# Kernel optimization log

Measured on AMD Instinct MI355X. Metric: run time of the kernel, lower is better.

## Reference

```python
import jax, jax.numpy as jnp
import numpy as np
from jax import lax

D = 1024  # input_dim
H = 1024  # hidden_dim
N = 32
T = 512


def setup_inputs() -> dict:
    key = jax.random.key(0)
    k1, k2, k3, k4 = jax.random.split(key, 4)
    std = 1.0 / np.sqrt(D + H)
    x = jax.random.normal(k1, (N, T, D), dtype=jnp.float32)
    state = jax.random.normal(k2, (N, H), dtype=jnp.float32)
    weight = jax.random.normal(k3, (D + H, 3 * (D + H)), dtype=jnp.float32) * std
    bias = jax.random.normal(k4, (3 * (D + H),), dtype=jnp.float32) * std
    return {"x": x, "state": state, "weight": weight, "bias": bias}


def reference(x, state, weight, bias):
    # weight slices, matching get_weights()
    Wxt = weight[:D, : 3 * H]            # (D, 3H)
    Wxd = weight[:D, 3 * H :]            # (D, 3D)
    Whd = weight[D:, 3 * H :]            # (H, 3D)
    Whtg = weight[D:, : 2 * H]           # (H, 2H)
    Whtc = weight[D:, 2 * H : 3 * H]     # (H, H)

    # temporal pre-activations: (N, T, 3H)
    gates = jnp.einsum('ntd,dk->ntk', x, Wxt) + bias[: 3 * H]

    def step(prev_ht, g_t):
        # g_t: (N, 3H)
        gg = jax.nn.sigmoid(g_t[:, : 2 * H] + prev_ht @ Whtg)
        u = gg[:, :H]
        r = gg[:, H:]
        hc = jnp.tanh(g_t[:, 2 * H :] + (r * prev_ht) @ Whtc)
        ht = prev_ht + u * (hc - prev_ht)
        return ht, ht

    final_ht, ht_seq = lax.scan(step, state, jnp.swapaxes(gates, 0, 1))
    ht = jnp.swapaxes(ht_seq, 0, 1)  # (N, T, H)

    # depth gates: bias + ht @ Whd everywhere; +x @ Wxd only on gate part
    gd = jnp.einsum('nth,hk->ntk', ht, Whd) + bias[3 * H :]       # (N, T, 3D)
    g2 = jax.nn.sigmoid(gd[..., : 2 * D] + jnp.einsum('ntd,dk->ntk', x, Wxd[:, : 2 * D]))
    ud = g2[..., :D]
    rd = g2[..., D:]
    hcd = jnp.tanh(gd[..., 2 * D :] + jnp.einsum('ntd,dk->ntk', rd * x, Wxd[:, 2 * D :]))
    h = x + ud * (hcd - x)
    return h, final_ht
```

## Files before the change

### kernel.cpp

```cpp
#include <hip/hip_runtime.h>
#include <cstdint>
#include <cstddef>

typedef unsigned int uint;
typedef unsigned short ushort;
typedef unsigned long long u64;
typedef __attribute__((ext_vector_type(8))) __bf16 bf16x8;
typedef __attribute__((ext_vector_type(4))) __bf16 bf16x4v;
typedef __attribute__((ext_vector_type(4))) float floatx4;

#define WLD 6144

static const size_t OFF_GATES = 0;
static const size_t OFF_XB    = 100663296;
static const size_t OFF_HTSEQ = 134217728;
static const size_t OFF_WHTGT = OFF_HTSEQ;
static const size_t OFF_WHTCT = OFF_HTSEQ + 4194304;
static const size_t OFF_WXTT  = 167772160;
static const size_t OFF_COMM  = OFF_WXTT;
static const size_t OFF_WHDT  = 174063616;
static const size_t OFF_WXD1T = 180355072;
static const size_t OFF_WXD2T = 184549376;

__device__ __forceinline__ float sigmoidf_(float x) { return 1.f / (1.f + __expf(-x)); }
__device__ __forceinline__ float tanhf_(float x) { float e = __expf(2.f * x); return 1.f - 2.f / (e + 1.f); }

__device__ __forceinline__ u64 ald64(const u64* p) {
  return __hip_atomic_load(p, __ATOMIC_RELAXED, __HIP_MEMORY_SCOPE_AGENT);
}
__device__ __forceinline__ void ast64(u64* p, u64 v) {
  __hip_atomic_store(p, v, __ATOMIC_RELAXED, __HIP_MEMORY_SCOPE_AGENT);
}
__device__ __forceinline__ ushort bfb(float v) {
  union { __bf16 b; ushort u; } t; t.b = (__bf16)v; return t.u;
}
__device__ __forceinline__ u64 pack4(float v) {
  ushort h = bfb(v);
  uint p2 = (uint)h | ((uint)(ushort)__shfl_xor((int)h, 1) << 16);
  u64 p4 = (u64)p2 | ((u64)(uint)__shfl_xor((int)p2, 2) << 32);
  return p4;
}


__global__ __launch_bounds__(256) void convert_x(const float4* __restrict__ x4,
                                                 __bf16* __restrict__ xb) {
  const int s = blockIdx.x;
  const int n = s >> 9, t = s & 511;
  const int d = (t << 5) | n;
  float4 v = x4[(size_t)s * 256 + threadIdx.x];
  bf16x4v o = { (__bf16)v.x, (__bf16)v.y, (__bf16)v.z, (__bf16)v.w };
  *reinterpret_cast<bf16x4v*>(xb + (size_t)d * 1024 + threadIdx.x * 4) = o;
}

__global__ __launch_bounds__(256) void zero_flags(u64* __restrict__ f) {
  ast64(f + (size_t)blockIdx.x * 256 + threadIdx.x, 0ull);
}

__global__ __launch_bounds__(256) void transpose_conv(const float* __restrict__ src,
                                                      __bf16* __restrict__ dst) {
  __shared__ float t[32][33];
  const int ct = blockIdx.x, kt = blockIdx.y;
  const int j = threadIdx.x & 31, ig = threadIdx.x >> 5;
#pragma unroll
  for (int ii = 0; ii < 4; ++ii) {
    int i = ig * 4 + ii;
    t[i][j] = src[(size_t)(kt * 32 + i) * WLD + ct * 32 + j];
  }
  __syncthreads();
#pragma unroll
  for (int ii = 0; ii < 4; ++ii) {
    int cc = ig * 4 + ii;
    dst[(size_t)(ct * 32 + cc) * 1024 + kt * 32 + j] = (__bf16)t[j][cc];
  }
}

template <int MODE>
__global__ __launch_bounds__(256) void gemm_bt(const __bf16* __restrict__ A, int lda,
                                               const __bf16* __restrict__ BT,
                                               const float* __restrict__ bias,
                                               __bf16* __restrict__ gbuf,
                                               const float* __restrict__ xf,
                                               float* __restrict__ hout, int ncols) {
  __shared__ __bf16 As[128][48];
  __shared__ __bf16 Bs[128][48];
  const int tid = threadIdx.x;
  const int lane = tid & 63, wave = tid >> 6;
  const int tm = blockIdx.y, tn = blockIdx.x;
  const int wm = (wave & 1) * 64, wn = (wave >> 1) * 64;
  floatx4 acc[4][4] = {};
  const int c = tid & 3, r0 = tid >> 2;
  const size_t arow = (size_t)tm * 128;
  const size_t brow = (size_t)tn * 128;

  for (int kk = 0; kk < 1024; kk += 32) {
    *reinterpret_cast<uint4*>(&As[r0][c * 8]) =
        *reinterpret_cast<const uint4*>(A + (arow + r0) * (size_t)lda + kk + c * 8);
    *reinterpret_cast<uint4*>(&As[r0 + 64][c * 8]) =
        *reinterpret_cast<const uint4*>(A + (arow + r0 + 64) * (size_t)lda + kk + c * 8);
    *reinterpret_cast<uint4*>(&Bs[r0][c * 8]) =
        *reinterpret_cast<const uint4*>(BT + (brow + r0) * 1024 + kk + c * 8);
    *reinterpret_cast<uint4*>(&Bs[r0 + 64][c * 8]) =
        *reinterpret_cast<const uint4*>(BT + (brow + r0 + 64) * 1024 + kk + c * 8);
    __syncthreads();
    const int mr = lane & 15, kg = (lane >> 4) * 8;
    bf16x8 af[4], bfr[4];
#pragma unroll
    for (int f = 0; f < 4; ++f) af[f] = *reinterpret_cast<const bf16x8*>(&As[wm + f * 16 + mr][kg]);
#pragma unroll
    for (int f = 0; f < 4; ++f) bfr[f] = *reinterpret_cast<const bf16x8*>(&Bs[wn + f * 16 + mr][kg]);
#pragma unroll
    for (int fi = 0; fi < 4; ++fi)
#pragma unroll
      for (int fj = 0; fj < 4; ++fj)
        acc[fi][fj] = __builtin_amdgcn_mfma_f32_16x16x32_bf16(af[fi], bfr[fj], acc[fi][fj], 0, 0, 0);
    __syncthreads();
  }

#pragma unroll
  for (int fi = 0; fi < 4; ++fi)
#pragma unroll
    for (int fj = 0; fj < 4; ++fj) {
      const int row0 = tm * 128 + wm + fi * 16 + (lane >> 4) * 4;
      const int col = tn * 128 + wn + fj * 16 + (lane & 15);
#pragma unroll
      for (int r = 0; r < 4; ++r) {
        const size_t row = (size_t)(row0 + r);
        float v = acc[fi][fj][r];
        if (MODE == 0 || MODE == 1) {
          gbuf[row * 3072 + col] = (__bf16)(v + bias[col]);
        } else if (MODE == 2) {
          float g = sigmoidf_(v + (float)gbuf[row * 3072 + col]);
          const size_t xrow = (size_t)(row & 31) * 512 + (row >> 5);
          if (col < 1024)
            gbuf[row * 3072 + col] = (__bf16)g;
          else
            gbuf[row * 3072 + col] = (__bf16)(g * xf[xrow * 1024 + (col - 1024)]);
        } else {
          float hcd = tanhf_(v + (float)gbuf[row * 3072 + 2048 + col]);
          float ud = (float)gbuf[row * 3072 + col];
          const size_t xrow = (size_t)(row & 31) * 512 + (row >> 5);
          float xv = xf[xrow * 1024 + col];
          hout[xrow * 1024 + col] = xv + ud * (hcd - xv);
        }
      }
    }
}

#define SMEM_BYTES 136960
#define WS 1032
__global__ __launch_bounds__(512) void recur_kernel(
    const __bf16* __restrict__ gates, const float* __restrict__ state,
    const __bf16* __restrict__ whtg_t, const __bf16* __restrict__ whtc_t,
    u64* __restrict__ ht_w, u64* __restrict__ rh_w,
    u64* __restrict__ fht, u64* __restrict__ frh,
    __bf16* __restrict__ htseq, float* __restrict__ otail) {
  extern __shared__ char smem[];
  __bf16* Wg  = (__bf16*)smem;
  __bf16* Wc  = (__bf16*)(smem + 66048);
  float*  red = (float*)(smem + 99072);
  float*  u_s = (float*)(smem + 132864);
  float*  hp_s= (float*)(smem + 134912);

  const int b = blockIdx.x, tid = threadIdx.x;
  const int lane = tid & 63, w = tid >> 6;
  const int mr = lane & 15, kq = lane >> 4;
  const int base0 = mr * 256 + w * 32 + kq * 2;
  const int base1 = (16 + mr) * 256 + w * 32 + kq * 2;

  for (int idx = tid; idx < 4096; idx += 512) {
    int row = idx >> 7, seg = idx & 127;
    int src = (row < 16) ? (b * 16 + row) : (1024 + b * 16 + row - 16);
    *reinterpret_cast<uint4*>(Wg + row * WS + seg * 8) =
        *reinterpret_cast<const uint4*>(whtg_t + (size_t)src * 1024 + seg * 8);
  }
  for (int idx = tid; idx < 2048; idx += 512) {
    int row = idx >> 7, seg = idx & 127;
    *reinterpret_cast<uint4*>(Wc + row * WS + seg * 8) =
        *reinterpret_cast<const uint4*>(whtc_t + (size_t)(b * 16 + row) * 1024 + seg * 8);
  }
  {
    int n = tid >> 4, cc = tid & 15;
    float sv = state[n * 1024 + b * 16 + cc];
    hp_s[n * 16 + cc] = sv;
    u64 p4 = pack4(sv);
    if (!(cc & 3)) ast64(ht_w + 8192 + n * 256 + b * 4 + (cc >> 2), p4);
  }
  __syncthreads();
  if (tid == 0) {
    asm volatile("s_waitcnt vmcnt(0)" ::: "memory");
    ast64(fht + b * 16, 1ull);
  }

  for (int t = 0; t < 512; ++t) {
    const uint e = (uint)t + 1u;
    const u64* htb = ht_w + (size_t)(e & 1) * 8192;
    u64*       rhb = rh_w + (size_t)(e & 1) * 8192;
    float hn_keep = 0.f;
    {
      __bf16 graw0, graw1;
      {
        int n = tid >> 5, col = tid & 31;
        int cc = (col < 16) ? (b * 16 + col) : (1024 + b * 16 + col - 16);
        graw0 = gates[(size_t)(t * 32 + n) * 3072 + cc];
        int o2 = tid + 512, n2 = o2 >> 5;
        graw1 = gates[(size_t)(t * 32 + n2) * 3072 + cc];
      }
      {
        const u64* fp = fht + (size_t)(w * 8 + (lane & 7)) * 16;
        bool rdy;
        do {
          u64 v = (lane < 8) ? ald64(fp) : (u64)e;
          rdy = (v >= (u64)e);
        } while (!__all(rdy));
        asm volatile("" ::: "memory");
      }
      u64 wa[4][2], wb[4][2];
#pragma unroll
      for (int c2 = 0; c2 < 4; ++c2) {
        wa[c2][0] = ald64(htb + base0 + c2 * 8);
        wa[c2][1] = ald64(htb + base0 + c2 * 8 + 1);
        wb[c2][0] = ald64(htb + base1 + c2 * 8);
        wb[c2][1] = ald64(htb + base1 + c2 * 8 + 1);
      }
      floatx4 acc[2][2] = {};
#pragma unroll
      for (int c2 = 0; c2 < 4; ++c2) {
        union { uint4 u; bf16x8 v; } fa, fb;
        fa.u = make_uint4((uint)wa[c2][0], (uint)(wa[c2][0] >> 32),
                          (uint)wa[c2][1], (uint)(wa[c2][1] >> 32));
        fb.u = make_uint4((uint)wb[c2][0], (uint)(wb[c2][0] >> 32),
                          (uint)wb[c2][1], (uint)(wb[c2][1] >> 32));
        const int kb = w * 128 + c2 * 32 + kq * 8;
        bf16x8 b0 = *reinterpret_cast<const bf16x8*>(Wg + mr * WS + kb);
        bf16x8 b1 = *reinterpret_cast<const bf16x8*>(Wg + (16 + mr) * WS + kb);
        acc[0][0] = __builtin_amdgcn_mfma_f32_16x16x32_bf16(fa.v, b0, acc[0][0], 0, 0, 0);
        acc[0][1] = __builtin_amdgcn_mfma_f32_16x16x32_bf16(fa.v, b1, acc[0][1], 0, 0, 0);
        acc[1][0] = __builtin_amdgcn_mfma_f32_16x16x32_bf16(fb.v, b0, acc[1][0], 0, 0, 0);
        acc[1][1] = __builtin_amdgcn_mfma_f32_16x16x32_bf16(fb.v, b1, acc[1][1], 0, 0, 0);
      }
#pragma unroll
      for (int ai = 0; ai < 2; ++ai)
#pragma unroll
        for (int cj = 0; cj < 2; ++cj)
#pragma unroll
          for (int r = 0; r < 4; ++r)
            red[w * 1056 + (ai * 16 + kq * 4 + r) * 33 + cj * 16 + mr] = acc[ai][cj][r];
      __syncthreads();
      {
        int n = tid >> 5, col = tid & 31;
        float s = 0.f;
#pragma unroll
        for (int w8 = 0; w8 < 8; ++w8) s += red[w8 * 1056 + n * 33 + col];
        float gg = sigmoidf_(s + (float)graw0);
        float pub = (col >= 16) ? gg * hp_s[n * 16 + (col - 16)] : 0.f;
        if (col < 16) u_s[n * 16 + col] = gg;
        u64 p4 = pack4(pub);
        if (col >= 16 && !(col & 3))
          ast64(rhb + n * 256 + b * 4 + ((col - 16) >> 2), p4);
        int o2 = tid + 512, n2 = o2 >> 5;
        float s2 = 0.f;
#pragma unroll
        for (int w8 = 0; w8 < 8; ++w8) s2 += red[w8 * 1056 + n2 * 33 + col];
        float gg2 = sigmoidf_(s2 + (float)graw1);
        float pub2 = (col >= 16) ? gg2 * hp_s[n2 * 16 + (col - 16)] : 0.f;
        if (col < 16) u_s[n2 * 16 + col] = gg2;
        u64 p42 = pack4(pub2);
        if (col >= 16 && !(col & 3))
          ast64(rhb + n2 * 256 + b * 4 + ((col - 16) >> 2), p42);
      }
      __syncthreads();
      if (tid == 0) {
        asm volatile("s_waitcnt vmcnt(0)" ::: "memory");
        ast64(frh + b * 16, (u64)e);
      }
    }
    {
      __bf16 gcraw;
      {
        int n = tid >> 4, col = tid & 15;
        gcraw = gates[(size_t)(t * 32 + n) * 3072 + 2048 + b * 16 + col];
      }
      {
        const u64* fp = frh + (size_t)(w * 8 + (lane & 7)) * 16;
        bool rdy;
        do {
          u64 v = (lane < 8) ? ald64(fp) : (u64)e;
          rdy = (v >= (u64)e);
        } while (!__all(rdy));
        asm volatile("" ::: "memory");
      }
      u64 wa[4][2], wb[4][2];
#pragma unroll
      for (int c2 = 0; c2 < 4; ++c2) {
        wa[c2][0] = ald64(rhb + base0 + c2 * 8);
        wa[c2][1] = ald64(rhb + base0 + c2 * 8 + 1);
        wb[c2][0] = ald64(rhb + base1 + c2 * 8);
        wb[c2][1] = ald64(rhb + base1 + c2 * 8 + 1);
      }
      floatx4 acc[2] = {};
#pragma unroll
      for (int c2 = 0; c2 < 4; ++c2) {
        union { uint4 u; bf16x8 v; } fa, fb;
        fa.u = make_uint4((uint)wa[c2][0], (uint)(wa[c2][0] >> 32),
                          (uint)wa[c2][1], (uint)(wa[c2][1] >> 32));
        fb.u = make_uint4((uint)wb[c2][0], (uint)(wb[c2][0] >> 32),
                          (uint)wb[c2][1], (uint)(wb[c2][1] >> 32));
        const int kb = w * 128 + c2 * 32 + kq * 8;
        bf16x8 bb = *reinterpret_cast<const bf16x8*>(Wc + mr * WS + kb);
        acc[0] = __builtin_amdgcn_mfma_f32_16x16x32_bf16(fa.v, bb, acc[0], 0, 0, 0);
        acc[1] = __builtin_amdgcn_mfma_f32_16x16x32_bf16(fb.v, bb, acc[1], 0, 0, 0);
      }
#pragma unroll
      for (int ai = 0; ai < 2; ++ai)
#pragma unroll
        for (int r = 0; r < 4; ++r)
          red[w * 1056 + (ai * 16 + kq * 4 + r) * 33 + mr] = acc[ai][r];
      __syncthreads();
      {
        int n = tid >> 4, col = tid & 15;
        float s = 0.f;
#pragma unroll
        for (int w8 = 0; w8 < 8; ++w8) s += red[w8 * 1056 + n * 33 + col];
        float hc = tanhf_(s + (float)gcraw);
        float hp = hp_s[n * 16 + col];
        float uu = u_s[n * 16 + col];
        float hn = hp + uu * (hc - hp);
        hp_s[n * 16 + col] = hn;
        hn_keep = hn;
        u64 p4 = pack4(hn);
        if (!(col & 3))
          ast64(ht_w + (size_t)((e + 1u) & 1) * 8192 + n * 256 + b * 4 + (col >> 2), p4);
      }
      __syncthreads();
      if (tid == 0) {
        asm volatile("s_waitcnt vmcnt(0)" ::: "memory");
        ast64(fht + b * 16, (u64)(e + 1u));
      }
      {
        int n = tid >> 4, col = tid & 15;
        htseq[(size_t)(t * 32 + n) * 1024 + b * 16 + col] = (__bf16)hn_keep;
        if (t == 511) otail[n * 1024 + b * 16 + col] = hn_keep;
      }
    }
  }
}


extern "C" void kernel_launch(void* const* d_in, const int* in_sizes, int n_in,
                              void* d_out, int out_size, void* d_ws, size_t ws_size,
                              hipStream_t stream) {
  const float* x = (const float*)d_in[0];
  const float* state = (const float*)d_in[1];
  const float* weight = (const float*)d_in[2];
  const float* bias = (const float*)d_in[3];
  float* out = (float*)d_out;
  char* ws = (char*)d_ws;

  __bf16* gates  = (__bf16*)(ws + OFF_GATES);
  __bf16* xb     = (__bf16*)(ws + OFF_XB);
  __bf16* htseq  = (__bf16*)(ws + OFF_HTSEQ);
  __bf16* whtg_t = (__bf16*)(ws + OFF_WHTGT);
  __bf16* whtc_t = (__bf16*)(ws + OFF_WHTCT);
  __bf16* wxtt   = (__bf16*)(ws + OFF_WXTT);
  __bf16* whdt   = (__bf16*)(ws + OFF_WHDT);
  __bf16* wxd1t  = (__bf16*)(ws + OFF_WXD1T);
  __bf16* wxd2t  = (__bf16*)(ws + OFF_WXD2T);
  u64*    comm   = (u64*)(ws + OFF_COMM);
  u64*    ht_w   = comm;
  u64*    rh_w   = comm + 16384;
  u64*    fht    = comm + 32768;
  u64*    frh    = comm + 33792;

  hipLaunchKernelGGL(convert_x, dim3(16384), dim3(256), 0, stream, (const float4*)x, xb);
  hipLaunchKernelGGL(transpose_conv, dim3(96, 32), dim3(256), 0, stream, weight, wxtt);
  hipLaunchKernelGGL(transpose_conv, dim3(64, 32), dim3(256), 0, stream, weight + 3072, wxd1t);
  hipLaunchKernelGGL(transpose_conv, dim3(32, 32), dim3(256), 0, stream, weight + 5120, wxd2t);
  hipLaunchKernelGGL(transpose_conv, dim3(96, 32), dim3(256), 0, stream,
                     weight + (size_t)1024 * WLD + 3072, whdt);
  hipLaunchKernelGGL(transpose_conv, dim3(64, 32), dim3(256), 0, stream,
                     weight + (size_t)1024 * WLD, whtg_t);
  hipLaunchKernelGGL(transpose_conv, dim3(32, 32), dim3(256), 0, stream,
                     weight + (size_t)1024 * WLD + 2048, whtc_t);

  hipLaunchKernelGGL((gemm_bt<0>), dim3(24, 128), dim3(256), 0, stream,
                     xb, 1024, wxtt, bias, gates, (const float*)nullptr, (float*)nullptr, 3072);

  hipLaunchKernelGGL(zero_flags, dim3(8), dim3(256), 0, stream, fht);

  {
    (void)hipFuncSetAttribute(reinterpret_cast<const void*>(recur_kernel),
                              hipFuncAttributeMaxDynamicSharedMemorySize, SMEM_BYTES);
    const __bf16* gatesc = gates;
    float* otail = out + 16777216;
    void* args[10];
    args[0] = (void*)&gatesc; args[1] = (void*)&state;  args[2] = (void*)&whtg_t;
    args[3] = (void*)&whtc_t; args[4] = (void*)&ht_w;   args[5] = (void*)&rh_w;
    args[6] = (void*)&fht;    args[7] = (void*)&frh;    args[8] = (void*)&htseq;
    args[9] = (void*)&otail;
    hipLaunchCooperativeKernel(recur_kernel, dim3(64), dim3(512), args, SMEM_BYTES, stream);
  }

  hipLaunchKernelGGL((gemm_bt<1>), dim3(24, 128), dim3(256), 0, stream,
                     htseq, 1024, whdt, bias + 3072, gates, (const float*)nullptr,
                     (float*)nullptr, 3072);
  hipLaunchKernelGGL((gemm_bt<2>), dim3(16, 128), dim3(256), 0, stream,
                     xb, 1024, wxd1t, bias, gates, x, (float*)nullptr, 2048);
  hipLaunchKernelGGL((gemm_bt<3>), dim3(8, 128), dim3(256), 0, stream,
                     gates + 1024, 3072, wxd2t, bias, gates, x, out, 1024);
}
```

Measured before the change: 6.239 ms.

## Use per-wave completion flags and register state in recurrent kernel

Replaces the per-block flag with per-wave flags, so each wave publishes its slice of h and r*h and signals independently. This removes two block-wide __syncthreads barriers per timestep, and consumers poll all 64 flags of the relevant blocks. Recurrent state (h, u) now lives in registers instead of shared memory. The 64-bit atomic loads are replaced with 128-bit coherent (sc0 sc1) inline-asm loads, and the flag area and zeroing are enlarged. The cost is more flag traffic and polling per step, and correctness now depends on the hand-written asm and explicit waitcnt ordering.

```diff
diff --git a/kernel.cpp b/kernel.cpp
--- a/kernel.cpp
+++ b/kernel.cpp
@@ -39,6 +39,10 @@
   uint p2 = (uint)h | ((uint)(ushort)__shfl_xor((int)h, 1) << 16);
   u64 p4 = (u64)p2 | ((u64)(uint)__shfl_xor((int)p2, 2) << 32);
   return p4;
+}
+union U4 { uint4 u; bf16x8 v; };
+__device__ __forceinline__ void ld16_cp(U4* dst, const u64* p) {
+  asm volatile("global_load_dwordx4 %0, %1, off sc0 sc1" : "=v"(dst->u) : "v"(p));
 }
 
 
@@ -146,7 +150,7 @@
     }
 }
 
-#define SMEM_BYTES 136960
+#define SMEM_BYTES 150272
 #define WS 1032
 __global__ __launch_bounds__(512) void recur_kernel(
     const __bf16* __restrict__ gates, const float* __restrict__ state,
@@ -155,17 +159,20 @@
     u64* __restrict__ fht, u64* __restrict__ frh,
     __bf16* __restrict__ htseq, float* __restrict__ otail) {
   extern __shared__ char smem[];
-  __bf16* Wg  = (__bf16*)smem;
-  __bf16* Wc  = (__bf16*)(smem + 66048);
-  float*  red = (float*)(smem + 99072);
-  float*  u_s = (float*)(smem + 132864);
-  float*  hp_s= (float*)(smem + 134912);
+  __bf16* Wg   = (__bf16*)smem;
+  __bf16* Wc   = (__bf16*)(smem + 66048);
+  float*  redA = (float*)(smem + 99072);
+  float*  redB = (float*)(smem + 132864);
 
   const int b = blockIdx.x, tid = threadIdx.x;
   const int lane = tid & 63, w = tid >> 6;
   const int mr = lane & 15, kq = lane >> 4;
+  const int n = 4 * w + kq;
+  const int c = mr;
   const int base0 = mr * 256 + w * 32 + kq * 2;
   const int base1 = (16 + mr) * 256 + w * 32 + kq * 2;
+  const u64* fpA = fht + ((size_t)(w * 8 + (lane >> 3)) * 8 + (lane & 7)) * 16;
+  const u64* fpB = frh + ((size_t)(w * 8 + (lane >> 3)) * 8 + (lane & 7)) * 16;
 
   for (int idx = tid; idx < 4096; idx += 512) {
     int row = idx >> 7, seg = idx & 127;
@@ -178,65 +185,42 @@
     *reinterpret_cast<uint4*>(Wc + row * WS + seg * 8) =
         *reinterpret_cast<const uint4*>(whtc_t + (size_t)(b * 16 + row) * 1024 + seg * 8);
   }
+  float hp_reg = state[n * 1024 + b * 16 + c];
+  float u_reg = 0.f;
   {
-    int n = tid >> 4, cc = tid & 15;
-    float sv = state[n * 1024 + b * 16 + cc];
-    hp_s[n * 16 + cc] = sv;
-    u64 p4 = pack4(sv);
-    if (!(cc & 3)) ast64(ht_w + 8192 + n * 256 + b * 4 + (cc >> 2), p4);
+    u64 p4 = pack4(hp_reg);
+    if (!(lane & 3)) ast64(ht_w + 8192 + n * 256 + b * 4 + (c >> 2), p4);
   }
   __syncthreads();
-  if (tid == 0) {
-    asm volatile("s_waitcnt vmcnt(0)" ::: "memory");
-    ast64(fht + b * 16, 1ull);
-  }
+  if (lane == 0) ast64(fht + (size_t)(b * 8 + w) * 16, 1ull);
 
   for (int t = 0; t < 512; ++t) {
     const uint e = (uint)t + 1u;
     const u64* htb = ht_w + (size_t)(e & 1) * 8192;
     u64*       rhb = rh_w + (size_t)(e & 1) * 8192;
-    float hn_keep = 0.f;
     {
-      __bf16 graw0, graw1;
-      {
-        int n = tid >> 5, col = tid & 31;
-        int cc = (col < 16) ? (b * 16 + col) : (1024 + b * 16 + col - 16);
-        graw0 = gates[(size_t)(t * 32 + n) * 3072 + cc];
-        int o2 = tid + 512, n2 = o2 >> 5;
-        graw1 = gates[(size_t)(t * 32 + n2) * 3072 + cc];
-      }
-      {
-        const u64* fp = fht + (size_t)(w * 8 + (lane & 7)) * 16;
-        bool rdy;
-        do {
-          u64 v = (lane < 8) ? ald64(fp) : (u64)e;
-          rdy = (v >= (u64)e);
-        } while (!__all(rdy));
-        asm volatile("" ::: "memory");
-      }
-      u64 wa[4][2], wb[4][2];
+      __bf16 graw_u = gates[(size_t)(t * 32 + n) * 3072 + b * 16 + c];
+      __bf16 graw_r = gates[(size_t)(t * 32 + n) * 3072 + 1024 + b * 16 + c];
+      while (!__all(ald64(fpA) >= (u64)e)) {}
+      asm volatile("" ::: "memory");
+      U4 wa[4], wb[4];
 #pragma unroll
       for (int c2 = 0; c2 < 4; ++c2) {
-        wa[c2][0] = ald64(htb + base0 + c2 * 8);
-        wa[c2][1] = ald64(htb + base0 + c2 * 8 + 1);
-        wb[c2][0] = ald64(htb + base1 + c2 * 8);
-        wb[c2][1] = ald64(htb + base1 + c2 * 8 + 1);
-      }
+        ld16_cp(&wa[c2], htb + base0 + c2 * 8);
+        ld16_cp(&wb[c2], htb + base1 + c2 * 8);
+      }
+      asm volatile("s_waitcnt vmcnt(0)" ::: "memory");
+      __builtin_amdgcn_sched_barrier(0);
       floatx4 acc[2][2] = {};
 #pragma unroll
       for (int c2 = 0; c2 < 4; ++c2) {
-        union { uint4 u; bf16x8 v; } fa, fb;
-        fa.u = make_uint4((uint)wa[c2][0], (uint)(wa[c2][0] >> 32),
-                          (uint)wa[c2][1], (uint)(wa[c2][1] >> 32));
-        fb.u = make_uint4((uint)wb[c2][0], (uint)(wb[c2][0] >> 32),
-                          (uint)wb[c2][1], (uint)(wb[c2][1] >> 32));
         const int kb = w * 128 + c2 * 32 + kq * 8;
         bf16x8 b0 = *reinterpret_cast<const bf16x8*>(Wg + mr * WS + kb);
         bf16x8 b1 = *reinterpret_cast<const bf16x8*>(Wg + (16 + mr) * WS + kb);
-        acc[0][0] = __builtin_amdgcn_mfma_f32_16x16x32_bf16(fa.v, b0, acc[0][0], 0, 0, 0);
-        acc[0][1] = __builtin_amdgcn_mfma_f32_16x16x32_bf16(fa.v, b1, acc[0][1], 0, 0, 0);
-        acc[1][0] = __builtin_amdgcn_mfma_f32_16x16x32_bf16(fb.v, b0, acc[1][0], 0, 0, 0);
-        acc[1][1] = __builtin_amdgcn_mfma_f32_16x16x32_bf16(fb.v, b1, acc[1][1], 0, 0, 0);
+        acc[0][0] = __builtin_amdgcn_mfma_f32_16x16x32_bf16(wa[c2].v, b0, acc[0][0], 0, 0, 0);
+        acc[0][1] = __builtin_amdgcn_mfma_f32_16x16x32_bf16(wa[c2].v, b1, acc[0][1], 0, 0, 0);
+        acc[1][0] = __builtin_amdgcn_mfma_f32_16x16x32_bf16(wb[c2].v, b0, acc[1][0], 0, 0, 0);
+        acc[1][1] = __builtin_amdgcn_mfma_f32_16x16x32_bf16(wb[c2].v, b1, acc[1][1], 0, 0, 0);
       }
 #pragma unroll
       for (int ai = 0; ai < 2; ++ai)
@@ -244,102 +228,64 @@
         for (int cj = 0; cj < 2; ++cj)
 #pragma unroll
           for (int r = 0; r < 4; ++r)
-            red[w * 1056 + (ai * 16 + kq * 4 + r) * 33 + cj * 16 + mr] = acc[ai][cj][r];
+            redA[w * 1056 + (ai * 16 + kq * 4 + r) * 33 + cj * 16 + mr] = acc[ai][cj][r];
       __syncthreads();
       {
-        int n = tid >> 5, col = tid & 31;
-        float s = 0.f;
-#pragma unroll
-        for (int w8 = 0; w8 < 8; ++w8) s += red[w8 * 1056 + n * 33 + col];
-        float gg = sigmoidf_(s + (float)graw0);
-        float pub = (col >= 16) ? gg * hp_s[n * 16 + (col - 16)] : 0.f;
-        if (col < 16) u_s[n * 16 + col] = gg;
+        float s1 = 0.f, s2 = 0.f;
+#pragma unroll
+        for (int w8 = 0; w8 < 8; ++w8) {
+          s1 += redA[w8 * 1056 + n * 33 + c];
+          s2 += redA[w8 * 1056 + n * 33 + 16 + c];
+        }
+        u_reg = sigmoidf_(s1 + (float)graw_u);
+        float gg_r = sigmoidf_(s2 + (float)graw_r);
+        float pub = gg_r * hp_reg;
         u64 p4 = pack4(pub);
-        if (col >= 16 && !(col & 3))
-          ast64(rhb + n * 256 + b * 4 + ((col - 16) >> 2), p4);
-        int o2 = tid + 512, n2 = o2 >> 5;
-        float s2 = 0.f;
-#pragma unroll
-        for (int w8 = 0; w8 < 8; ++w8) s2 += red[w8 * 1056 + n2 * 33 + col];
-        float gg2 = sigmoidf_(s2 + (float)graw1);
-        float pub2 = (col >= 16) ? gg2 * hp_s[n2 * 16 + (col - 16)] : 0.f;
-        if (col < 16) u_s[n2 * 16 + col] = gg2;
-        u64 p42 = pack4(pub2);
-        if (col >= 16 && !(col & 3))
-          ast64(rhb + n2 * 256 + b * 4 + ((col - 16) >> 2), p42);
-      }
-      __syncthreads();
-      if (tid == 0) {
-        asm volatile("s_waitcnt vmcnt(0)" ::: "memory");
-        ast64(frh + b * 16, (u64)e);
-      }
+        if (!(lane & 3)) ast64(rhb + n * 256 + b * 4 + (c >> 2), p4);
+      }
+      asm volatile("s_waitcnt vmcnt(0)" ::: "memory");
+      if (lane == 0) ast64(frh + (size_t)(b * 8 + w) * 16, (u64)e);
     }
     {
-      __bf16 gcraw;
-      {
-        int n = tid >> 4, col = tid & 15;
-        gcraw = gates[(size_t)(t * 32 + n) * 3072 + 2048 + b * 16 + col];
-      }
-      {
-        const u64* fp = frh + (size_t)(w * 8 + (lane & 7)) * 16;
-        bool rdy;
-        do {
-          u64 v = (lane < 8) ? ald64(fp) : (u64)e;
-          rdy = (v >= (u64)e);
-        } while (!__all(rdy));
-        asm volatile("" ::: "memory");
-      }
-      u64 wa[4][2], wb[4][2];
+      __bf16 gcraw = gates[(size_t)(t * 32 + n) * 3072 + 2048 + b * 16 + c];
+      while (!__all(ald64(fpB) >= (u64)e)) {}
+      asm volatile("" ::: "memory");
+      U4 wa[4], wb[4];
 #pragma unroll
       for (int c2 = 0; c2 < 4; ++c2) {
-        wa[c2][0] = ald64(rhb + base0 + c2 * 8);
-        wa[c2][1] = ald64(rhb + base0 + c2 * 8 + 1);
-        wb[c2][0] = ald64(rhb + base1 + c2 * 8);
-        wb[c2][1] = ald64(rhb + base1 + c2 * 8 + 1);
-      }
+        ld16_cp(&wa[c2], rhb + base0 + c2 * 8);
+        ld16_cp(&wb[c2], rhb + base1 + c2 * 8);
+      }
+      asm volatile("s_waitcnt vmcnt(0)" ::: "memory");
+      __builtin_amdgcn_sched_barrier(0);
       floatx4 acc[2] = {};
 #pragma unroll
       for (int c2 = 0; c2 < 4; ++c2) {
-        union { uint4 u; bf16x8 v; } fa, fb;
-        fa.u = make_uint4((uint)wa[c2][0], (uint)(wa[c2][0] >> 32),
-                          (uint)wa[c2][1], (uint)(wa[c2][1] >> 32));
-        fb.u = make_uint4((uint)wb[c2][0], (uint)(wb[c2][0] >> 32),
-                          (uint)wb[c2][1], (uint)(wb[c2][1] >> 32));
         const int kb = w * 128 + c2 * 32 + kq * 8;
         bf16x8 bb = *reinterpret_cast<const bf16x8*>(Wc + mr * WS + kb);
-        acc[0] = __builtin_amdgcn_mfma_f32_16x16x32_bf16(fa.v, bb, acc[0], 0, 0, 0);
-        acc[1] = __builtin_amdgcn_mfma_f32_16x16x32_bf16(fb.v, bb, acc[1], 0, 0, 0);
+        acc[0] = __builtin_amdgcn_mfma_f32_16x16x32_bf16(wa[c2].v, bb, acc[0], 0, 0, 0);
+        acc[1] = __builtin_amdgcn_mfma_f32_16x16x32_bf16(wb[c2].v, bb, acc[1], 0, 0, 0);
       }
 #pragma unroll
       for (int ai = 0; ai < 2; ++ai)
 #pragma unroll
         for (int r = 0; r < 4; ++r)
-          red[w * 1056 + (ai * 16 + kq * 4 + r) * 33 + mr] = acc[ai][r];
+          redB[w * 544 + (ai * 16 + kq * 4 + r) * 17 + mr] = acc[ai][r];
       __syncthreads();
       {
-        int n = tid >> 4, col = tid & 15;
         float s = 0.f;
 #pragma unroll
-        for (int w8 = 0; w8 < 8; ++w8) s += red[w8 * 1056 + n * 33 + col];
+        for (int w8 = 0; w8 < 8; ++w8) s += redB[w8 * 544 + n * 17 + c];
         float hc = tanhf_(s + (float)gcraw);
-        float hp = hp_s[n * 16 + col];
-        float uu = u_s[n * 16 + col];
-        float hn = hp + uu * (hc - hp);
-        hp_s[n * 16 + col] = hn;
-        hn_keep = hn;
+        float hn = hp_reg + u_reg * (hc - hp_reg);
+        hp_reg = hn;
         u64 p4 = pack4(hn);
-        if (!(col & 3))
-          ast64(ht_w + (size_t)((e + 1u) & 1) * 8192 + n * 256 + b * 4 + (col >> 2), p4);
-      }
-      __syncthreads();
-      if (tid == 0) {
+        if (!(lane & 3))
+          ast64(ht_w + (size_t)((e + 1u) & 1) * 8192 + n * 256 + b * 4 + (c >> 2), p4);
         asm volatile("s_waitcnt vmcnt(0)" ::: "memory");
-        ast64(fht + b * 16, (u64)(e + 1u));
-      }
-      {
-        int n = tid >> 4, col = tid & 15;
-        htseq[(size_t)(t * 32 + n) * 1024 + b * 16 + col] = (__bf16)hn_keep;
-        if (t == 511) otail[n * 1024 + b * 16 + col] = hn_keep;
+        if (lane == 0) ast64(fht + (size_t)(b * 8 + w) * 16, (u64)(e + 1u));
+        htseq[(size_t)(t * 32 + n) * 1024 + b * 16 + c] = (__bf16)hn;
+        if (t == 511) otail[n * 1024 + b * 16 + c] = hn;
       }
     }
   }
@@ -369,7 +315,7 @@
   u64*    ht_w   = comm;
   u64*    rh_w   = comm + 16384;
   u64*    fht    = comm + 32768;
-  u64*    frh    = comm + 33792;
+  u64*    frh    = comm + 40960;
 
   hipLaunchKernelGGL(convert_x, dim3(16384), dim3(256), 0, stream, (const float4*)x, xb);
   hipLaunchKernelGGL(transpose_conv, dim3(96, 32), dim3(256), 0, stream, weight, wxtt);
@@ -385,7 +331,7 @@
   hipLaunchKernelGGL((gemm_bt<0>), dim3(24, 128), dim3(256), 0, stream,
                      xb, 1024, wxtt, bias, gates, (const float*)nullptr, (float*)nullptr, 3072);
 
-  hipLaunchKernelGGL(zero_flags, dim3(8), dim3(256), 0, stream, fht);
+  hipLaunchKernelGGL(zero_flags, dim3(64), dim3(256), 0, stream, fht);
 
   {
     (void)hipFuncSetAttribute(reinterpret_cast<const void*>(recur_kernel),
```

New measurement: 5.709 ms. -8.5%, faster.
